# Performance work log

Measured on AMD Instinct MI355X. Metric: run time of the kernel, lower is better.

The kernel has to match this reference:

```python
import jax, jax.numpy as jnp
import numpy as np

HEADS = 8
WS = 8  # window size


def conv1x1(x, w, b):
    # x: [B,C,H,W], w: [Cout,Cin], b: [Cout]
    return jnp.einsum('bchw,oc->bohw', x, w) + b[None, :, None, None]


def to_windows(x, heads, ws):
    # x: [B,C,H,W] -> [B*nH*nW, heads, ws*ws, C//heads]
    B, C, H, W = x.shape
    d = C // heads
    x = x.reshape(B, heads, d, H // ws, ws, W // ws, ws)
    x = x.transpose(0, 3, 5, 1, 4, 6, 2)  # B, nH, nW, heads, ws, ws, d
    return x.reshape(B * (H // ws) * (W // ws), heads, ws * ws, d)


def from_windows(xw, B, C, H, W, heads, ws):
    d = C // heads
    x = xw.reshape(B, H // ws, W // ws, heads, ws, ws, d)
    x = x.transpose(0, 3, 6, 1, 4, 2, 5)  # B, heads, d, nH, ws, nW, ws
    return x.reshape(B, C, H, W)


def setup_inputs() -> dict:
    key = jax.random.key(0)
    ks = jax.random.split(key, 10)
    B, C, H, W = 4, 256, 256, 256
    s = 0.02
    return {
        'q_feat': jax.random.normal(ks[0], (B, C, H, W), jnp.float32),
        'kv_feat': jax.random.normal(ks[1], (B, C, H, W), jnp.float32),
        'wq': jax.random.normal(ks[2], (C, C), jnp.float32) * s,
        'bq': jnp.zeros((C,), jnp.float32),
        'wk': jax.random.normal(ks[3], (C, C), jnp.float32) * s,
        'bk': jnp.zeros((C,), jnp.float32),
        'wv': jax.random.normal(ks[4], (C, C), jnp.float32) * s,
        'bv': jnp.zeros((C,), jnp.float32),
        'wp': jax.random.normal(ks[5], (C, C), jnp.float32) * s,
        'bp': jnp.zeros((C,), jnp.float32),
    }


def reference(q_feat, kv_feat, wq, bq, wk, bk, wv, bv, wp, bp):
    B, C, H, W = q_feat.shape
    heads, ws = HEADS, WS
    scale = (C // heads) ** (-0.5)

    q = to_windows(conv1x1(q_feat, wq, bq), heads, ws)   # [Nw, h, ws*ws, d]
    k = to_windows(conv1x1(kv_feat, wk, bk), heads, ws)
    v = to_windows(conv1x1(kv_feat, wv, bv), heads, ws)

    attn = jnp.einsum('whqd,whkd->whqk', q, k) * scale
    attn = jax.nn.softmax(attn, axis=-1)
    out_w = jnp.einsum('whqk,whkd->whqd', attn, v)

    out = from_windows(out_w, B, C, H, W, heads, ws)
    return conv1x1(out, wp, bp)
```

## Files before the change

### kernel.cpp

```cpp
#include <hip/hip_runtime.h>
#include <cstdint>
#include <cstddef>


typedef __attribute__((ext_vector_type(8))) short bfx8;
typedef __attribute__((ext_vector_type(4))) float f32x4;

#define HW 65536
#define NC 256
#define QKV_STRIDE 16777216UL

__device__ __forceinline__ unsigned short f2bf(float f) {
  union { float f; unsigned u; } v; v.f = f;
  unsigned r = v.u + 0x7FFFu + ((v.u >> 16) & 1u);
  return (unsigned short)(r >> 16);
}

__device__ __forceinline__ unsigned xswz(unsigned n) {
  return ((n ^ (n >> 2)) & 7u) << 4;
}

__global__ __launch_bounds__(256) void prep_weights(
    const float* __restrict__ wq, const float* __restrict__ wk,
    const float* __restrict__ wv, const float* __restrict__ wp,
    unsigned short* __restrict__ dst) {
  int i = blockIdx.x * 256 + threadIdx.x;
  int e = i & 7, lane = (i >> 3) & 63, ks = (i >> 9) & 7, ot = i >> 12;
  int src = (ot * 16 + (lane & 15)) * 256 + ks * 32 + (lane >> 4) * 8 + e;
  dst[i]          = f2bf(wq[src]);
  dst[i + 65536]  = f2bf(wk[src]);
  dst[i + 131072] = f2bf(wv[src]);
  dst[i + 196608] = f2bf(wp[src]);
}

__device__ __forceinline__ void gemm_pass(
    const unsigned short* __restrict__ wT, const unsigned char* __restrict__ smem,
    int wid, int lane, int g, int qh, f32x4 (&acc)[4][4]) {
#pragma unroll
  for (int i = 0; i < 4; ++i)
#pragma unroll
    for (int j = 0; j < 4; ++j) acc[i][j] = (f32x4){0.f, 0.f, 0.f, 0.f};

  bfx8 afr[4];
#pragma unroll
  for (int mt = 0; mt < 4; ++mt)
    afr[mt] = *(const bfx8*)(wT + (((wid * 4 + mt) * 8 + 0) * 64 + lane) * 8);

  for (int ks = 0; ks < 8; ++ks) {
    bfx8 naf[4];
    if (ks < 7) {
#pragma unroll
      for (int mt = 0; mt < 4; ++mt)
        naf[mt] = *(const bfx8*)(wT + (((wid * 4 + mt) * 8 + ks + 1) * 64 + lane) * 8);
    }
#pragma unroll
    for (int nt = 0; nt < 4; ++nt) {
      unsigned n = (unsigned)(nt * 16 + qh);
      unsigned byte = (n * 512 + (unsigned)(ks * 64 + g * 16)) ^ xswz(n);
      bfx8 bfr = *(const bfx8*)(smem + byte);
#pragma unroll
      for (int mt = 0; mt < 4; ++mt)
        acc[mt][nt] = __builtin_amdgcn_mfma_f32_16x16x32_bf16(afr[mt], bfr, acc[mt][nt], 0, 0, 0);
    }
    if (ks < 7) {
#pragma unroll
      for (int mt = 0; mt < 4; ++mt) afr[mt] = naf[mt];
    }
  }
}

__device__ __forceinline__ void store_qk(
    const f32x4 (&acc)[4][4], const float* __restrict__ bias,
    unsigned short* __restrict__ outw, int n0, int wid, int g, int qh) {
  const int h_img = n0 >> 8, w0b = n0 & 255;
#pragma unroll
  for (int mt = 0; mt < 4; ++mt) {
    int o = wid * 64 + mt * 16 + g * 4;
    f32x4 bb = *(const f32x4*)&bias[o];
    int head = o >> 5, dbase = o & 31;
#pragma unroll
    for (int nt = 0; nt < 4; ++nt) {
      int n = nt * 16 + qh;
      int w_img = w0b + n;
      int win = ((h_img >> 3) << 5) + (w_img >> 3);
      int pos = ((h_img & 7) << 3) + (w_img & 7);
      f32x4 a = acc[mt][nt];
      uint2 pv;
      pv.x = (unsigned)f2bf(a.x + bb.x) | ((unsigned)f2bf(a.y + bb.y) << 16);
      pv.y = (unsigned)f2bf(a.z + bb.z) | ((unsigned)f2bf(a.w + bb.w) << 16);
      *(uint2*)&outw[((size_t)(win * 8 + head) * 64 + pos) * 32 + dbase] = pv;
    }
  }
}

__global__ __launch_bounds__(256) void qkv_gemm(
    const float* __restrict__ xq, const float* __restrict__ xkv,
    const unsigned short* __restrict__ wbf,
    const float* __restrict__ bq, const float* __restrict__ bk,
    const float* __restrict__ bv,
    unsigned short* __restrict__ q_w, unsigned short* __restrict__ k_w,
    unsigned short* __restrict__ v_w, int batch0, int batched) {
  __shared__ __align__(16) unsigned char smem[36864];

  const int tid = threadIdx.x;
  const int lane = tid & 63;
  const int wid = tid >> 6;
  const int g = lane >> 4;
  const int qh = lane & 15;
  const int mode = blockIdx.x & 1;
  const int n0 = (int)(blockIdx.x >> 1) * 64;
  const int batch = batch0 + blockIdx.z;
  const size_t qofs = batched ? (size_t)blockIdx.z * QKV_STRIDE : 0;
  const float* x = (mode ? xkv : xq) + (size_t)batch * NC * HW;

  {
    const int n4 = lane & 15;
    const int c8a = wid * 4 + (lane >> 4);
    const float* xp0 = x + (size_t)(c8a * 8) * HW + n0 + n4 * 4;
    const float* xp1 = xp0 + (size_t)128 * HW;
    f32x4 r0[8], r1[8];
#pragma unroll
    for (int i = 0; i < 8; ++i) r0[i] = *(const f32x4*)(xp0 + (size_t)i * HW);
#pragma unroll
    for (int i = 0; i < 8; ++i) r1[i] = *(const f32x4*)(xp1 + (size_t)i * HW);
#pragma unroll
    for (int e = 0; e < 4; ++e) {
      unsigned n = (unsigned)(n4 * 4 + e);
      uint4 u;
      u.x = (unsigned)f2bf(r0[0][e]) | ((unsigned)f2bf(r0[1][e]) << 16);
      u.y = (unsigned)f2bf(r0[2][e]) | ((unsigned)f2bf(r0[3][e]) << 16);
      u.z = (unsigned)f2bf(r0[4][e]) | ((unsigned)f2bf(r0[5][e]) << 16);
      u.w = (unsigned)f2bf(r0[6][e]) | ((unsigned)f2bf(r0[7][e]) << 16);
      *(uint4*)(smem + ((n * 512 + (unsigned)c8a * 16) ^ xswz(n))) = u;
      uint4 v;
      v.x = (unsigned)f2bf(r1[0][e]) | ((unsigned)f2bf(r1[1][e]) << 16);
      v.y = (unsigned)f2bf(r1[2][e]) | ((unsigned)f2bf(r1[3][e]) << 16);
      v.z = (unsigned)f2bf(r1[4][e]) | ((unsigned)f2bf(r1[5][e]) << 16);
      v.w = (unsigned)f2bf(r1[6][e]) | ((unsigned)f2bf(r1[7][e]) << 16);
      *(uint4*)(smem + ((n * 512 + (unsigned)(c8a + 16) * 16) ^ xswz(n))) = v;
    }
  }
  __syncthreads();

  f32x4 acc[4][4];
  if (mode == 0) {
    gemm_pass(wbf, smem, wid, lane, g, qh, acc);
    store_qk(acc, bq, q_w + qofs, n0, wid, g, qh);
  } else {
    gemm_pass(wbf + 65536, smem, wid, lane, g, qh, acc);
    store_qk(acc, bk, k_w + qofs, n0, wid, g, qh);
    gemm_pass(wbf + 131072, smem, wid, lane, g, qh, acc);
    __syncthreads();
    unsigned short* Vt = (unsigned short*)smem;
#pragma unroll
    for (int mt = 0; mt < 4; ++mt) {
      int o = wid * 64 + mt * 16 + g * 4;
      f32x4 bb = *(const f32x4*)&bv[o];
#pragma unroll
      for (int nt = 0; nt < 4; ++nt) {
        int n = nt * 16 + qh;
        f32x4 a = acc[mt][nt];
        Vt[(o + 0) * 72 + n] = f2bf(a.x + bb.x);
        Vt[(o + 1) * 72 + n] = f2bf(a.y + bb.y);
        Vt[(o + 2) * 72 + n] = f2bf(a.z + bb.z);
        Vt[(o + 3) * 72 + n] = f2bf(a.w + bb.w);
      }
    }
    __syncthreads();
    const int h_img = n0 >> 8, w0b = n0 & 255;
    unsigned short* vw = v_w + qofs;
#pragma unroll
    for (int it = 0; it < 8; ++it) {
      int id = it * 256 + tid;
      int o = id >> 3, oct = id & 7;
      uint4 val = *(const uint4*)&Vt[o * 72 + oct * 8];
      int head = o >> 5, dd = o & 31;
      int win = ((h_img >> 3) << 5) + (w0b >> 3) + oct;
      *(uint4*)&vw[((size_t)(win * 8 + head) * 32 + dd) * 64 + ((h_img & 7) << 3)] = val;
    }
  }
}

__global__ __launch_bounds__(256) void attn_conv(
    const unsigned short* __restrict__ q_w, const unsigned short* __restrict__ k_w,
    const unsigned short* __restrict__ v_w, const unsigned short* __restrict__ wpT,
    const float* __restrict__ bp, float* __restrict__ out, int batch0, int batched) {
  __shared__ unsigned short P_lds[4][2048];
  __shared__ unsigned short y_t[16384];

  const int tid = threadIdx.x;
  const int lane = tid & 63;
  const int wid = tid >> 6;
  const int g = lane >> 4;
  const int qh = lane & 15;
  const int bid = blockIdx.x;
  const int winl = ((bid & 7) << 7) | (bid >> 3);
  const int batch = batch0 + blockIdx.z;
  const size_t qofs = batched ? (size_t)blockIdx.z * QKV_STRIDE : 0;
  const float scale = 0.17677669529663687f;

  char* pbase = (char*)&P_lds[wid][0];

#pragma unroll
  for (int hi = 0; hi < 2; ++hi) {
    const int head = wid + hi * 4;
    const unsigned short* qb = q_w + qofs + (size_t)(winl * 8 + head) * 2048;
    const unsigned short* kb = k_w + qofs + (size_t)(winl * 8 + head) * 2048;
    const unsigned short* vb = v_w + qofs + (size_t)(winl * 8 + head) * 2048;

    bfx8 kf[4], qf[4];
#pragma unroll
    for (int t = 0; t < 4; ++t) {
      kf[t] = *(const bfx8*)(kb + (t * 16 + qh) * 32 + g * 8);
      qf[t] = *(const bfx8*)(qb + (t * 16 + qh) * 32 + g * 8);
    }
    f32x4 zero = {0.f, 0.f, 0.f, 0.f};
    f32x4 st[4][4];
#pragma unroll
    for (int kt = 0; kt < 4; ++kt)
#pragma unroll
      for (int qt = 0; qt < 4; ++qt)
        st[kt][qt] = __builtin_amdgcn_mfma_f32_16x16x32_bf16(kf[kt], qf[qt], zero, 0, 0, 0);

    float rv[4];
#pragma unroll
    for (int qt = 0; qt < 4; ++qt) {
      float m = -1e30f;
#pragma unroll
      for (int kt = 0; kt < 4; ++kt) {
        f32x4 v = st[kt][qt];
        m = fmaxf(m, fmaxf(fmaxf(v.x, v.y), fmaxf(v.z, v.w)));
      }
      m = fmaxf(m, __shfl_xor(m, 16, 64));
      m = fmaxf(m, __shfl_xor(m, 32, 64));
      float ssum = 0.f;
#pragma unroll
      for (int kt = 0; kt < 4; ++kt) {
        f32x4 v = st[kt][qt], e;
        e.x = __expf((v.x - m) * scale);
        e.y = __expf((v.y - m) * scale);
        e.z = __expf((v.z - m) * scale);
        e.w = __expf((v.w - m) * scale);
        ssum += e.x + e.y + e.z + e.w;
        st[kt][qt] = e;
      }
      ssum += __shfl_xor(ssum, 16, 64);
      ssum += __shfl_xor(ssum, 32, 64);
      rv[qt] = 1.f / ssum;
    }

    f32x4 ot[2][4];
#pragma unroll
    for (int dt = 0; dt < 2; ++dt)
#pragma unroll
      for (int qt = 0; qt < 4; ++qt) ot[dt][qt] = zero;

#pragma unroll
    for (int s = 0; s < 2; ++s) {
#pragma unroll
      for (int qt = 0; qt < 4; ++qt) {
        int q = qt * 16 + qh;
        unsigned sw = ((unsigned)(q & 3)) << 4;
        float r = rv[qt];
#pragma unroll
        for (int k2 = 0; k2 < 2; ++k2) {
          f32x4 e = st[s * 2 + k2][qt];
          uint2 pv;
          pv.x = (unsigned)f2bf(e.x * r) | ((unsigned)f2bf(e.y * r) << 16);
          pv.y = (unsigned)f2bf(e.z * r) | ((unsigned)f2bf(e.w * r) << 16);
          unsigned byte = ((unsigned)q * 64 + (unsigned)(k2 * 32 + g * 8)) ^ sw;
          *(uint2*)(pbase + byte) = pv;
        }
      }
      bfx8 pf[4];
#pragma unroll
      for (int qt = 0; qt < 4; ++qt) {
        int q = qt * 16 + qh;
        unsigned byte = ((unsigned)q * 64 + (unsigned)(g * 16)) ^ (((unsigned)(q & 3)) << 4);
        pf[qt] = *(const bfx8*)(pbase + byte);
      }
#pragma unroll
      for (int dt = 0; dt < 2; ++dt) {
        bfx8 vf = *(const bfx8*)(vb + (dt * 16 + qh) * 64 + s * 32 + g * 8);
#pragma unroll
        for (int qt = 0; qt < 4; ++qt)
          ot[dt][qt] = __builtin_amdgcn_mfma_f32_16x16x32_bf16(vf, pf[qt], ot[dt][qt], 0, 0, 0);
      }
    }

#pragma unroll
    for (int dt = 0; dt < 2; ++dt) {
      int cb = head * 32 + dt * 16 + g * 4;
#pragma unroll
      for (int qt = 0; qt < 4; ++qt) {
        int pos = qt * 16 + qh;
        f32x4 a = ot[dt][qt];
        uint2 pv;
        pv.x = (unsigned)f2bf(a.x) | ((unsigned)f2bf(a.y) << 16);
        pv.y = (unsigned)f2bf(a.z) | ((unsigned)f2bf(a.w) << 16);
        unsigned byte = ((unsigned)pos * 512 + (unsigned)cb * 2) ^ (((unsigned)(pos & 7)) << 4);
        *(uint2*)((char*)y_t + byte) = pv;
      }
    }
  }
  __syncthreads();

  f32x4 acc[4][4];
#pragma unroll
  for (int i = 0; i < 4; ++i)
#pragma unroll
    for (int j = 0; j < 4; ++j) acc[i][j] = (f32x4){0.f, 0.f, 0.f, 0.f};

  for (int ks = 0; ks < 8; ++ks) {
    bfx8 af[4];
#pragma unroll
    for (int mt = 0; mt < 4; ++mt)
      af[mt] = *(const bfx8*)(wpT + (((wid * 4 + mt) * 8 + ks) * 64 + lane) * 8);
#pragma unroll
    for (int nt = 0; nt < 4; ++nt) {
      int pos = nt * 16 + qh;
      unsigned byte = ((unsigned)pos * 512 + (unsigned)(ks * 64 + g * 16)) ^ (((unsigned)(pos & 7)) << 4);
      bfx8 bfr = *(const bfx8*)((char*)y_t + byte);
#pragma unroll
      for (int mt = 0; mt < 4; ++mt)
        acc[mt][nt] = __builtin_amdgcn_mfma_f32_16x16x32_bf16(af[mt], bfr, acc[mt][nt], 0, 0, 0);
    }
  }

  const int wrow = winl >> 5, wcol = winl & 31;
  float* ob_ = out + (size_t)batch * NC * HW;
#pragma unroll
  for (int mt = 0; mt < 4; ++mt) {
    int o0 = wid * 64 + mt * 16 + g * 4;
    float b0 = bp[o0], b1 = bp[o0 + 1], b2 = bp[o0 + 2], b3 = bp[o0 + 3];
#pragma unroll
    for (int nt = 0; nt < 4; ++nt) {
      int pos = nt * 16 + qh;
      int h_img = wrow * 8 + (pos >> 3);
      int w_img = wcol * 8 + (pos & 7);
      float* pp = ob_ + (size_t)o0 * HW + h_img * 256 + w_img;
      pp[0]      = acc[mt][nt].x + b0;
      pp[HW]     = acc[mt][nt].y + b1;
      pp[2 * HW] = acc[mt][nt].z + b2;
      pp[3 * HW] = acc[mt][nt].w + b3;
    }
  }
}

extern "C" void kernel_launch(void* const* d_in, const int* in_sizes, int n_in,
                              void* d_out, int out_size, void* d_ws, size_t ws_size,
                              hipStream_t stream) {
  const float* q_feat = (const float*)d_in[0];
  const float* kv_feat = (const float*)d_in[1];
  const float* wq = (const float*)d_in[2];
  const float* bq = (const float*)d_in[3];
  const float* wk = (const float*)d_in[4];
  const float* bk = (const float*)d_in[5];
  const float* wv = (const float*)d_in[6];
  const float* bv = (const float*)d_in[7];
  const float* wp = (const float*)d_in[8];
  const float* bp = (const float*)d_in[9];
  float* out = (float*)d_out;

  unsigned short* wbf = (unsigned short*)d_ws;
  const size_t need_batched = 524288ul + 12ul * QKV_STRIDE * 2ul;

  hipLaunchKernelGGL(prep_weights, dim3(256), dim3(256), 0, stream, wq, wk, wv, wp, wbf);

  if (ws_size >= need_batched) {
    unsigned short* q_w = wbf + 262144;
    unsigned short* k_w = q_w + 4 * QKV_STRIDE;
    unsigned short* v_w = k_w + 4 * QKV_STRIDE;
    hipLaunchKernelGGL(qkv_gemm, dim3(2048, 1, 4), dim3(256), 0, stream,
                       q_feat, kv_feat, wbf, bq, bk, bv, q_w, k_w, v_w, 0, 1);
    hipLaunchKernelGGL(attn_conv, dim3(1024, 1, 4), dim3(256), 0, stream,
                       q_w, k_w, v_w, wbf + 196608, bp, out, 0, 1);
  } else {
    unsigned short* q_w = wbf + 262144;
    unsigned short* k_w = q_w + QKV_STRIDE;
    unsigned short* v_w = k_w + QKV_STRIDE;
    for (int b = 0; b < 4; ++b) {
      hipLaunchKernelGGL(qkv_gemm, dim3(2048, 1, 1), dim3(256), 0, stream,
                         q_feat, kv_feat, wbf, bq, bk, bv, q_w, k_w, v_w, b, 0);
      hipLaunchKernelGGL(attn_conv, dim3(1024, 1, 1), dim3(256), 0, stream,
                         q_w, k_w, v_w, wbf + 196608, bp, out, b, 0);
    }
  }
}
```

Before: 645.2 us.

## Make qkv_gemm persistent over four tiles per row with double-buffered LDS prefetch

Each qkv_gemm block now handles a full 256-pixel image row as four 64-pixel tiles instead of one, with grid size cut by four. The fp32 activation loads for the next tile are issued into registers before the current tile's GEMM, then converted to bf16 and packed into the alternate LDS buffer, which overlaps global memory latency with MFMA work. The V transpose staging is reworked to a per-wave region inside the current buffer so it can reuse the LDS, and launch bounds request two blocks per CU. The cost is higher register pressure from holding the prefetched registers alongside the accumulators, plus fewer blocks to spread across CUs.

```diff
diff --git a/kernel.cpp b/kernel.cpp
--- a/kernel.cpp
+++ b/kernel.cpp
@@ -93,14 +93,14 @@
   }
 }
 
-__global__ __launch_bounds__(256) void qkv_gemm(
+__global__ __launch_bounds__(256, 2) void qkv_gemm(
     const float* __restrict__ xq, const float* __restrict__ xkv,
     const unsigned short* __restrict__ wbf,
     const float* __restrict__ bq, const float* __restrict__ bk,
     const float* __restrict__ bv,
     unsigned short* __restrict__ q_w, unsigned short* __restrict__ k_w,
     unsigned short* __restrict__ v_w, int batch0, int batched) {
-  __shared__ __align__(16) unsigned char smem[36864];
+  __shared__ __align__(16) unsigned char smem[2][32768];
 
   const int tid = threadIdx.x;
   const int lane = tid & 63;
@@ -108,21 +108,24 @@
   const int g = lane >> 4;
   const int qh = lane & 15;
   const int mode = blockIdx.x & 1;
-  const int n0 = (int)(blockIdx.x >> 1) * 64;
+  const int row = (int)(blockIdx.x >> 1);
   const int batch = batch0 + blockIdx.z;
   const size_t qofs = batched ? (size_t)blockIdx.z * QKV_STRIDE : 0;
   const float* x = (mode ? xkv : xq) + (size_t)batch * NC * HW;
 
-  {
-    const int n4 = lane & 15;
-    const int c8a = wid * 4 + (lane >> 4);
-    const float* xp0 = x + (size_t)(c8a * 8) * HW + n0 + n4 * 4;
-    const float* xp1 = xp0 + (size_t)128 * HW;
-    f32x4 r0[8], r1[8];
-#pragma unroll
-    for (int i = 0; i < 8; ++i) r0[i] = *(const f32x4*)(xp0 + (size_t)i * HW);
-#pragma unroll
-    for (int i = 0; i < 8; ++i) r1[i] = *(const f32x4*)(xp1 + (size_t)i * HW);
+  const int n4 = lane & 15;
+  const int c8a = wid * 4 + (lane >> 4);
+  const float* xb0 = x + (size_t)(c8a * 8) * HW + row * 256 + n4 * 4;
+  const float* xb1 = xb0 + (size_t)128 * HW;
+
+  f32x4 r0[8], r1[8];
+  auto issue = [&](int t) {
+#pragma unroll
+    for (int i = 0; i < 8; ++i) r0[i] = *(const f32x4*)(xb0 + (size_t)i * HW + t * 64);
+#pragma unroll
+    for (int i = 0; i < 8; ++i) r1[i] = *(const f32x4*)(xb1 + (size_t)i * HW + t * 64);
+  };
+  auto pack = [&](unsigned char* dst) {
 #pragma unroll
     for (int e = 0; e < 4; ++e) {
       unsigned n = (unsigned)(n4 * 4 + e);
@@ -131,52 +134,71 @@
       u.y = (unsigned)f2bf(r0[2][e]) | ((unsigned)f2bf(r0[3][e]) << 16);
       u.z = (unsigned)f2bf(r0[4][e]) | ((unsigned)f2bf(r0[5][e]) << 16);
       u.w = (unsigned)f2bf(r0[6][e]) | ((unsigned)f2bf(r0[7][e]) << 16);
-      *(uint4*)(smem + ((n * 512 + (unsigned)c8a * 16) ^ xswz(n))) = u;
+      *(uint4*)(dst + ((n * 512 + (unsigned)c8a * 16) ^ xswz(n))) = u;
       uint4 v;
       v.x = (unsigned)f2bf(r1[0][e]) | ((unsigned)f2bf(r1[1][e]) << 16);
       v.y = (unsigned)f2bf(r1[2][e]) | ((unsigned)f2bf(r1[3][e]) << 16);
       v.z = (unsigned)f2bf(r1[4][e]) | ((unsigned)f2bf(r1[5][e]) << 16);
       v.w = (unsigned)f2bf(r1[6][e]) | ((unsigned)f2bf(r1[7][e]) << 16);
-      *(uint4*)(smem + ((n * 512 + (unsigned)(c8a + 16) * 16) ^ xswz(n))) = v;
-    }
-  }
-  __syncthreads();
-
-  f32x4 acc[4][4];
-  if (mode == 0) {
-    gemm_pass(wbf, smem, wid, lane, g, qh, acc);
-    store_qk(acc, bq, q_w + qofs, n0, wid, g, qh);
-  } else {
-    gemm_pass(wbf + 65536, smem, wid, lane, g, qh, acc);
-    store_qk(acc, bk, k_w + qofs, n0, wid, g, qh);
-    gemm_pass(wbf + 131072, smem, wid, lane, g, qh, acc);
+      *(uint4*)(dst + ((n * 512 + (unsigned)(c8a + 16) * 16) ^ xswz(n))) = v;
+    }
+  };
+
+  issue(0);
+  pack(smem[0]);
+
+  for (int t = 0; t < 4; ++t) {
+    unsigned char* cur = smem[t & 1];
+    unsigned char* alt = smem[(t + 1) & 1];
     __syncthreads();
-    unsigned short* Vt = (unsigned short*)smem;
-#pragma unroll
-    for (int mt = 0; mt < 4; ++mt) {
-      int o = wid * 64 + mt * 16 + g * 4;
-      f32x4 bb = *(const f32x4*)&bv[o];
-#pragma unroll
-      for (int nt = 0; nt < 4; ++nt) {
-        int n = nt * 16 + qh;
-        f32x4 a = acc[mt][nt];
-        Vt[(o + 0) * 72 + n] = f2bf(a.x + bb.x);
-        Vt[(o + 1) * 72 + n] = f2bf(a.y + bb.y);
-        Vt[(o + 2) * 72 + n] = f2bf(a.z + bb.z);
-        Vt[(o + 3) * 72 + n] = f2bf(a.w + bb.w);
-      }
-    }
-    __syncthreads();
-    const int h_img = n0 >> 8, w0b = n0 & 255;
-    unsigned short* vw = v_w + qofs;
-#pragma unroll
-    for (int it = 0; it < 8; ++it) {
-      int id = it * 256 + tid;
-      int o = id >> 3, oct = id & 7;
-      uint4 val = *(const uint4*)&Vt[o * 72 + oct * 8];
-      int head = o >> 5, dd = o & 31;
-      int win = ((h_img >> 3) << 5) + (w0b >> 3) + oct;
-      *(uint4*)&vw[((size_t)(win * 8 + head) * 32 + dd) * 64 + ((h_img & 7) << 3)] = val;
+    if (t < 3) issue(t + 1);
+    const int n0t = row * 256 + t * 64;
+    f32x4 acc[4][4];
+    if (mode == 0) {
+      gemm_pass(wbf, cur, wid, lane, g, qh, acc);
+      store_qk(acc, bq, q_w + qofs, n0t, wid, g, qh);
+      if (t < 3) pack(alt);
+    } else {
+      gemm_pass(wbf + 65536, cur, wid, lane, g, qh, acc);
+      store_qk(acc, bk, k_w + qofs, n0t, wid, g, qh);
+      f32x4 vacc[4][4];
+      gemm_pass(wbf + 131072, cur, wid, lane, g, qh, vacc);
+      if (t < 3) pack(alt);
+      __syncthreads();
+      unsigned short* Vw = (unsigned short*)(void*)cur + wid * 2304;
+#pragma unroll
+      for (int s2 = 0; s2 < 2; ++s2) {
+#pragma unroll
+        for (int mi = 0; mi < 2; ++mi) {
+          int mt = s2 * 2 + mi;
+          int o = wid * 64 + mt * 16 + g * 4;
+          f32x4 bb = *(const f32x4*)&bv[o];
+          int od = mi * 16 + g * 4;
+#pragma unroll
+          for (int nt = 0; nt < 4; ++nt) {
+            int n = nt * 16 + qh;
+            f32x4 a = vacc[mt][nt];
+            Vw[(od + 0) * 72 + n] = f2bf(a.x + bb.x);
+            Vw[(od + 1) * 72 + n] = f2bf(a.y + bb.y);
+            Vw[(od + 2) * 72 + n] = f2bf(a.z + bb.z);
+            Vw[(od + 3) * 72 + n] = f2bf(a.w + bb.w);
+          }
+        }
+        {
+          int o_loc = lane >> 1, half = lane & 1;
+          int o = wid * 64 + s2 * 32 + o_loc;
+          int head = o >> 5, dd = o & 31;
+#pragma unroll
+          for (int c = 0; c < 4; ++c) {
+            int n = half * 32 + c * 8;
+            uint4 val = *(const uint4*)&Vw[o_loc * 72 + n];
+            int w_img = t * 64 + n;
+            int win = ((row >> 3) << 5) + (w_img >> 3);
+            *(uint4*)&v_w[qofs + ((size_t)(win * 8 + head) * 32 + dd) * 64 +
+                          ((row & 7) << 3)] = val;
+          }
+        }
+      }
     }
   }
 }
@@ -371,7 +393,7 @@
     unsigned short* q_w = wbf + 262144;
     unsigned short* k_w = q_w + 4 * QKV_STRIDE;
     unsigned short* v_w = k_w + 4 * QKV_STRIDE;
-    hipLaunchKernelGGL(qkv_gemm, dim3(2048, 1, 4), dim3(256), 0, stream,
+    hipLaunchKernelGGL(qkv_gemm, dim3(512, 1, 4), dim3(256), 0, stream,
                        q_feat, kv_feat, wbf, bq, bk, bv, q_w, k_w, v_w, 0, 1);
     hipLaunchKernelGGL(attn_conv, dim3(1024, 1, 4), dim3(256), 0, stream,
                        q_w, k_w, v_w, wbf + 196608, bp, out, 0, 1);
@@ -380,7 +402,7 @@
     unsigned short* k_w = q_w + QKV_STRIDE;
     unsigned short* v_w = k_w + QKV_STRIDE;
     for (int b = 0; b < 4; ++b) {
-      hipLaunchKernelGGL(qkv_gemm, dim3(2048, 1, 1), dim3(256), 0, stream,
+      hipLaunchKernelGGL(qkv_gemm, dim3(512, 1, 1), dim3(256), 0, stream,
                          q_feat, kv_feat, wbf, bq, bk, bv, q_w, k_w, v_w, b, 0);
       hipLaunchKernelGGL(attn_conv, dim3(1024, 1, 1), dim3(256), 0, stream,
                          q_w, k_w, v_w, wbf + 196608, bp, out, b, 0);
```

Measured after the change: 966.7 us. 1.5x slower.

## Keep projection weights in registers and tile QKV GEMM by attention window

Applied to the files above, without the earlier changes.

The QKV projection kernel now launches one block per (batch, mode, window-row strip) instead of one per 64-pixel tile. Each block loads its 256x256 bf16 weight slice into registers once, then loops over 8 window-aligned 8x8 pixel tiles. Tiles now cover whole windows, so the Q/K/V outputs are written as contiguous per-window chunks, and K and V are computed by separate blocks rather than sharing one staged input tile. In exchange, the key/value input is read twice, each global load covers only short 32-byte row segments, and register pressure rises under a two-blocks-per-CU launch bound.

```diff
diff --git a/kernel.cpp b/kernel.cpp
--- a/kernel.cpp
+++ b/kernel.cpp
@@ -33,67 +33,7 @@
   dst[i + 196608] = f2bf(wp[src]);
 }
 
-__device__ __forceinline__ void gemm_pass(
-    const unsigned short* __restrict__ wT, const unsigned char* __restrict__ smem,
-    int wid, int lane, int g, int qh, f32x4 (&acc)[4][4]) {
-#pragma unroll
-  for (int i = 0; i < 4; ++i)
-#pragma unroll
-    for (int j = 0; j < 4; ++j) acc[i][j] = (f32x4){0.f, 0.f, 0.f, 0.f};
-
-  bfx8 afr[4];
-#pragma unroll
-  for (int mt = 0; mt < 4; ++mt)
-    afr[mt] = *(const bfx8*)(wT + (((wid * 4 + mt) * 8 + 0) * 64 + lane) * 8);
-
-  for (int ks = 0; ks < 8; ++ks) {
-    bfx8 naf[4];
-    if (ks < 7) {
-#pragma unroll
-      for (int mt = 0; mt < 4; ++mt)
-        naf[mt] = *(const bfx8*)(wT + (((wid * 4 + mt) * 8 + ks + 1) * 64 + lane) * 8);
-    }
-#pragma unroll
-    for (int nt = 0; nt < 4; ++nt) {
-      unsigned n = (unsigned)(nt * 16 + qh);
-      unsigned byte = (n * 512 + (unsigned)(ks * 64 + g * 16)) ^ xswz(n);
-      bfx8 bfr = *(const bfx8*)(smem + byte);
-#pragma unroll
-      for (int mt = 0; mt < 4; ++mt)
-        acc[mt][nt] = __builtin_amdgcn_mfma_f32_16x16x32_bf16(afr[mt], bfr, acc[mt][nt], 0, 0, 0);
-    }
-    if (ks < 7) {
-#pragma unroll
-      for (int mt = 0; mt < 4; ++mt) afr[mt] = naf[mt];
-    }
-  }
-}
-
-__device__ __forceinline__ void store_qk(
-    const f32x4 (&acc)[4][4], const float* __restrict__ bias,
-    unsigned short* __restrict__ outw, int n0, int wid, int g, int qh) {
-  const int h_img = n0 >> 8, w0b = n0 & 255;
-#pragma unroll
-  for (int mt = 0; mt < 4; ++mt) {
-    int o = wid * 64 + mt * 16 + g * 4;
-    f32x4 bb = *(const f32x4*)&bias[o];
-    int head = o >> 5, dbase = o & 31;
-#pragma unroll
-    for (int nt = 0; nt < 4; ++nt) {
-      int n = nt * 16 + qh;
-      int w_img = w0b + n;
-      int win = ((h_img >> 3) << 5) + (w_img >> 3);
-      int pos = ((h_img & 7) << 3) + (w_img & 7);
-      f32x4 a = acc[mt][nt];
-      uint2 pv;
-      pv.x = (unsigned)f2bf(a.x + bb.x) | ((unsigned)f2bf(a.y + bb.y) << 16);
-      pv.y = (unsigned)f2bf(a.z + bb.z) | ((unsigned)f2bf(a.w + bb.w) << 16);
-      *(uint2*)&outw[((size_t)(win * 8 + head) * 64 + pos) * 32 + dbase] = pv;
-    }
-  }
-}
-
-__global__ __launch_bounds__(256) void qkv_gemm(
+__global__ __launch_bounds__(256, 2) void qkv_gemm(
     const float* __restrict__ xq, const float* __restrict__ xkv,
     const unsigned short* __restrict__ wbf,
     const float* __restrict__ bq, const float* __restrict__ bk,
@@ -107,76 +47,124 @@
   const int wid = tid >> 6;
   const int g = lane >> 4;
   const int qh = lane & 15;
-  const int mode = blockIdx.x & 1;
-  const int n0 = (int)(blockIdx.x >> 1) * 64;
-  const int batch = batch0 + blockIdx.z;
-  const size_t qofs = batched ? (size_t)blockIdx.z * QKV_STRIDE : 0;
+
+  const int bid = blockIdx.x;
+  const int mode = bid % 3;
+  const int strip = bid / 3;
+  const int batch = batch0 + (strip >> 7);
+  const int rem = strip & 127;
+  const int r0 = (rem >> 2) * 8;
+  const int oc = rem & 3;
+  const int wrow = rem >> 2;
+
   const float* x = (mode ? xkv : xq) + (size_t)batch * NC * HW;
-
-  {
-    const int n4 = lane & 15;
-    const int c8a = wid * 4 + (lane >> 4);
-    const float* xp0 = x + (size_t)(c8a * 8) * HW + n0 + n4 * 4;
-    const float* xp1 = xp0 + (size_t)128 * HW;
-    f32x4 r0[8], r1[8];
-#pragma unroll
-    for (int i = 0; i < 8; ++i) r0[i] = *(const f32x4*)(xp0 + (size_t)i * HW);
-#pragma unroll
-    for (int i = 0; i < 8; ++i) r1[i] = *(const f32x4*)(xp1 + (size_t)i * HW);
+  const unsigned short* wT = wbf + mode * 65536;
+  const float* bias = mode == 0 ? bq : (mode == 1 ? bk : bv);
+  unsigned short* outw =
+      (mode == 0 ? q_w : (mode == 1 ? k_w : v_w)) +
+      (batched ? (size_t)(batch - batch0) * QKV_STRIDE : 0);
+
+  bfx8 wreg[4][8];
+#pragma unroll
+  for (int mt = 0; mt < 4; ++mt)
+#pragma unroll
+    for (int ks = 0; ks < 8; ++ks)
+      wreg[mt][ks] = *(const bfx8*)(wT + (((wid * 4 + mt) * 8 + ks) * 64 + lane) * 8);
+
+  const int cg = tid >> 4;
+  const int rr = (tid >> 1) & 7;
+  const int wh = tid & 1;
+  const float* xb = x + (size_t)(cg * 16) * HW + (r0 + rr) * 256 + oc * 64 + wh * 4;
+
+  for (int t = 0; t < 8; ++t) {
+    const int win = wrow * 32 + oc * 8 + t;
+
+    f32x4 ld[16];
+#pragma unroll
+    for (int i = 0; i < 16; ++i)
+      ld[i] = *(const f32x4*)(xb + (size_t)i * HW + t * 8);
+
+    __syncthreads();
+
 #pragma unroll
     for (int e = 0; e < 4; ++e) {
-      unsigned n = (unsigned)(n4 * 4 + e);
-      uint4 u;
-      u.x = (unsigned)f2bf(r0[0][e]) | ((unsigned)f2bf(r0[1][e]) << 16);
-      u.y = (unsigned)f2bf(r0[2][e]) | ((unsigned)f2bf(r0[3][e]) << 16);
-      u.z = (unsigned)f2bf(r0[4][e]) | ((unsigned)f2bf(r0[5][e]) << 16);
-      u.w = (unsigned)f2bf(r0[6][e]) | ((unsigned)f2bf(r0[7][e]) << 16);
-      *(uint4*)(smem + ((n * 512 + (unsigned)c8a * 16) ^ xswz(n))) = u;
-      uint4 v;
-      v.x = (unsigned)f2bf(r1[0][e]) | ((unsigned)f2bf(r1[1][e]) << 16);
-      v.y = (unsigned)f2bf(r1[2][e]) | ((unsigned)f2bf(r1[3][e]) << 16);
-      v.z = (unsigned)f2bf(r1[4][e]) | ((unsigned)f2bf(r1[5][e]) << 16);
-      v.w = (unsigned)f2bf(r1[6][e]) | ((unsigned)f2bf(r1[7][e]) << 16);
-      *(uint4*)(smem + ((n * 512 + (unsigned)(c8a + 16) * 16) ^ xswz(n))) = v;
-    }
-  }
-  __syncthreads();
-
-  f32x4 acc[4][4];
-  if (mode == 0) {
-    gemm_pass(wbf, smem, wid, lane, g, qh, acc);
-    store_qk(acc, bq, q_w + qofs, n0, wid, g, qh);
-  } else {
-    gemm_pass(wbf + 65536, smem, wid, lane, g, qh, acc);
-    store_qk(acc, bk, k_w + qofs, n0, wid, g, qh);
-    gemm_pass(wbf + 131072, smem, wid, lane, g, qh, acc);
+      unsigned n = (unsigned)(rr * 8 + wh * 4 + e);
+      unsigned base = n * 512 + (unsigned)cg * 32;
+      uint4 u0, u1;
+      u0.x = (unsigned)f2bf(ld[0][e]) | ((unsigned)f2bf(ld[1][e]) << 16);
+      u0.y = (unsigned)f2bf(ld[2][e]) | ((unsigned)f2bf(ld[3][e]) << 16);
+      u0.z = (unsigned)f2bf(ld[4][e]) | ((unsigned)f2bf(ld[5][e]) << 16);
+      u0.w = (unsigned)f2bf(ld[6][e]) | ((unsigned)f2bf(ld[7][e]) << 16);
+      u1.x = (unsigned)f2bf(ld[8][e]) | ((unsigned)f2bf(ld[9][e]) << 16);
+      u1.y = (unsigned)f2bf(ld[10][e]) | ((unsigned)f2bf(ld[11][e]) << 16);
+      u1.z = (unsigned)f2bf(ld[12][e]) | ((unsigned)f2bf(ld[13][e]) << 16);
+      u1.w = (unsigned)f2bf(ld[14][e]) | ((unsigned)f2bf(ld[15][e]) << 16);
+      *(uint4*)(smem + (base ^ xswz(n))) = u0;
+      *(uint4*)(smem + ((base + 16) ^ xswz(n))) = u1;
+    }
     __syncthreads();
-    unsigned short* Vt = (unsigned short*)smem;
-#pragma unroll
-    for (int mt = 0; mt < 4; ++mt) {
-      int o = wid * 64 + mt * 16 + g * 4;
-      f32x4 bb = *(const f32x4*)&bv[o];
+
+    f32x4 acc[4][4];
+#pragma unroll
+    for (int i = 0; i < 4; ++i)
+#pragma unroll
+      for (int j = 0; j < 4; ++j) acc[i][j] = (f32x4){0.f, 0.f, 0.f, 0.f};
+
+    for (int ks = 0; ks < 8; ++ks) {
 #pragma unroll
       for (int nt = 0; nt < 4; ++nt) {
-        int n = nt * 16 + qh;
-        f32x4 a = acc[mt][nt];
-        Vt[(o + 0) * 72 + n] = f2bf(a.x + bb.x);
-        Vt[(o + 1) * 72 + n] = f2bf(a.y + bb.y);
-        Vt[(o + 2) * 72 + n] = f2bf(a.z + bb.z);
-        Vt[(o + 3) * 72 + n] = f2bf(a.w + bb.w);
-      }
-    }
-    __syncthreads();
-    const int h_img = n0 >> 8, w0b = n0 & 255;
-    unsigned short* vw = v_w + qofs;
-#pragma unroll
-    for (int it = 0; it < 8; ++it) {
-      int id = it * 256 + tid;
-      int o = id >> 3, oct = id & 7;
-      uint4 val = *(const uint4*)&Vt[o * 72 + oct * 8];
-      int head = o >> 5, dd = o & 31;
-      int win = ((h_img >> 3) << 5) + (w0b >> 3) + oct;
-      *(uint4*)&vw[((size_t)(win * 8 + head) * 32 + dd) * 64 + ((h_img & 7) << 3)] = val;
+        unsigned n = (unsigned)(nt * 16 + qh);
+        unsigned byte = (n * 512 + (unsigned)(ks * 64 + g * 16)) ^ xswz(n);
+        bfx8 bfr = *(const bfx8*)(smem + byte);
+#pragma unroll
+        for (int mt = 0; mt < 4; ++mt)
+          acc[mt][nt] = __builtin_amdgcn_mfma_f32_16x16x32_bf16(wreg[mt][ks], bfr, acc[mt][nt], 0, 0, 0);
+      }
+    }
+
+    if (mode != 2) {
+#pragma unroll
+      for (int mt = 0; mt < 4; ++mt) {
+        int o = wid * 64 + mt * 16 + g * 4;
+        f32x4 bb = *(const f32x4*)&bias[o];
+        int head = o >> 5, dbase = o & 31;
+        unsigned short* wb_ = outw + (size_t)(win * 8 + head) * 2048;
+#pragma unroll
+        for (int nt = 0; nt < 4; ++nt) {
+          int pos = nt * 16 + qh;
+          f32x4 a = acc[mt][nt];
+          uint2 pv;
+          pv.x = (unsigned)f2bf(a.x + bb.x) | ((unsigned)f2bf(a.y + bb.y) << 16);
+          pv.y = (unsigned)f2bf(a.z + bb.z) | ((unsigned)f2bf(a.w + bb.w) << 16);
+          *(uint2*)&wb_[pos * 32 + dbase] = pv;
+        }
+      }
+    } else {
+      __syncthreads();
+      unsigned short* Vt = (unsigned short*)smem;
+#pragma unroll
+      for (int mt = 0; mt < 4; ++mt) {
+        int o = wid * 64 + mt * 16 + g * 4;
+        f32x4 bb = *(const f32x4*)&bias[o];
+#pragma unroll
+        for (int nt = 0; nt < 4; ++nt) {
+          int n = nt * 16 + qh;
+          f32x4 a = acc[mt][nt];
+          Vt[(o + 0) * 72 + n] = f2bf(a.x + bb.x);
+          Vt[(o + 1) * 72 + n] = f2bf(a.y + bb.y);
+          Vt[(o + 2) * 72 + n] = f2bf(a.z + bb.z);
+          Vt[(o + 3) * 72 + n] = f2bf(a.w + bb.w);
+        }
+      }
+      __syncthreads();
+#pragma unroll
+      for (int it = 0; it < 8; ++it) {
+        int id = it * 256 + tid;
+        int o = id >> 3, oct = id & 7;
+        uint4 val = *(const uint4*)&Vt[o * 72 + oct * 8];
+        int head = o >> 5, dd = o & 31;
+        *(uint4*)&outw[((size_t)(win * 8 + head) * 32 + dd) * 64 + oct * 8] = val;
+      }
     }
   }
 }
@@ -371,7 +359,7 @@
     unsigned short* q_w = wbf + 262144;
     unsigned short* k_w = q_w + 4 * QKV_STRIDE;
     unsigned short* v_w = k_w + 4 * QKV_STRIDE;
-    hipLaunchKernelGGL(qkv_gemm, dim3(2048, 1, 4), dim3(256), 0, stream,
+    hipLaunchKernelGGL(qkv_gemm, dim3(1536), dim3(256), 0, stream,
                        q_feat, kv_feat, wbf, bq, bk, bv, q_w, k_w, v_w, 0, 1);
     hipLaunchKernelGGL(attn_conv, dim3(1024, 1, 4), dim3(256), 0, stream,
                        q_w, k_w, v_w, wbf + 196608, bp, out, 0, 1);
@@ -380,7 +368,7 @@
     unsigned short* k_w = q_w + QKV_STRIDE;
     unsigned short* v_w = k_w + QKV_STRIDE;
     for (int b = 0; b < 4; ++b) {
-      hipLaunchKernelGGL(qkv_gemm, dim3(2048, 1, 1), dim3(256), 0, stream,
+      hipLaunchKernelGGL(qkv_gemm, dim3(384), dim3(256), 0, stream,
                          q_feat, kv_feat, wbf, bq, bk, bv, q_w, k_w, v_w, b, 0);
       hipLaunchKernelGGL(attn_conv, dim3(1024, 1, 1), dim3(256), 0, stream,
                          q_w, k_w, v_w, wbf + 196608, bp, out, b, 0);
```

Measured after the change: 810.7 us. 25.6% more time.
